# Kernel tuning notes

Measured on AMD Instinct MI355X. Metric: run time of the kernel, lower is better.

Reference implementation:

```python
import jax, jax.numpy as jnp
import numpy as np

N_SYM, N_DIS, F_IN, HID, OUT, E = 50000, 10000, 128, 128, 64, 640000
NEG_SLOPE = 0.2


def _gat(x_src, x_dst, src, dst, Ws, Wd, a_s, a_d, b, n_dst):
    # PyG GATConv (bipartite, heads=1, add_self_loops=False)
    h_src = x_src @ Ws                      # [Ns, H]
    h_dst = x_dst @ Wd                      # [Nd, H]
    al = h_src @ a_s                        # [Ns]
    ar = h_dst @ a_d                        # [Nd]
    e = jax.nn.leaky_relu(al[src] + ar[dst], NEG_SLOPE)   # [E]
    m = jax.ops.segment_max(e, dst, num_segments=n_dst)   # per-dst max
    ex = jnp.exp(e - m[dst])
    den = jax.ops.segment_sum(ex, dst, num_segments=n_dst)
    alpha = ex / den[dst]                   # segment softmax over in-edges
    out = jax.ops.segment_sum(alpha[:, None] * h_src[src], dst, num_segments=n_dst)
    return out + b


def setup_inputs() -> dict:
    key = jax.random.key(0)
    ks = jax.random.split(key, 16)
    s = 0.05
    return {
        'x_sym': jax.random.normal(ks[0], (N_SYM, F_IN), jnp.float32),
        'x_dis': jax.random.normal(ks[1], (N_DIS, F_IN), jnp.float32),
        'edge_src': jax.random.randint(ks[2], (E,), 0, N_SYM, jnp.int32),
        'edge_dst': jax.random.randint(ks[3], (E,), 0, N_DIS, jnp.int32),
        'Wsrc_sd': jax.random.normal(ks[4], (F_IN, HID), jnp.float32) * s,
        'Wdst_sd': jax.random.normal(ks[5], (F_IN, HID), jnp.float32) * s,
        'asrc_sd': jax.random.normal(ks[6], (HID,), jnp.float32) * s,
        'adst_sd': jax.random.normal(ks[7], (HID,), jnp.float32) * s,
        'b_sd': jax.random.normal(ks[8], (HID,), jnp.float32) * s,
        'Wsrc_ds': jax.random.normal(ks[9], (F_IN, HID), jnp.float32) * s,
        'Wdst_ds': jax.random.normal(ks[10], (F_IN, HID), jnp.float32) * s,
        'asrc_ds': jax.random.normal(ks[11], (HID,), jnp.float32) * s,
        'adst_ds': jax.random.normal(ks[12], (HID,), jnp.float32) * s,
        'b_ds': jax.random.normal(ks[13], (HID,), jnp.float32) * s,
        'lin_W': jax.random.normal(ks[14], (HID, OUT), jnp.float32) * s,
        'lin_b': jax.random.normal(ks[15], (OUT,), jnp.float32) * s,
    }


def reference(x_sym, x_dis, edge_src, edge_dst,
              Wsrc_sd, Wdst_sd, asrc_sd, adst_sd, b_sd,
              Wsrc_ds, Wdst_ds, asrc_ds, adst_ds, b_ds,
              lin_W, lin_b):
    # symptom -> disease edge type
    h_dis = _gat(x_sym, x_dis, edge_src, edge_dst,
                 Wsrc_sd, Wdst_sd, asrc_sd, adst_sd, b_sd, N_DIS)
    # disease -> symptom (reverse edges)
    h_sym = _gat(x_dis, x_sym, edge_dst, edge_src,
                 Wsrc_ds, Wdst_ds, asrc_ds, adst_ds, b_ds, N_SYM)
    h_sym = jax.nn.relu(h_sym)  # only symptom branch feeds lin
    return h_sym @ lin_W + lin_b
```

## Files before the change

### kernel.cpp

```cpp
#include <hip/hip_runtime.h>
#include <hip/hip_fp16.h>

#define N_SYM 50000
#define N_DIS 10000
#define F_IN 128
#define HID 128
#define OUTF 64
#define NE 640000
#define NEG_SLOPE 0.2f

#define SPAN 128
#define NB 391
#define SUBS 16
#define SCAP 192
#define CURSTRIDE 16
#define NREG (NB * SUBS)
#define LCAP 48

typedef _Float16 f16x8 __attribute__((ext_vector_type(8)));
typedef float f32x4 __attribute__((ext_vector_type(4)));

#define R1 16
__global__ __launch_bounds__(256) void k_proj(const float* __restrict__ x,
                                              const float* __restrict__ W,
                                              const float* __restrict__ asrc,
                                              const float* __restrict__ Wd,
                                              const float* __restrict__ ad,
                                              __half* __restrict__ h,
                                              float* __restrict__ al2,
                                              float* __restrict__ v_dst,
                                              int* __restrict__ bcur) {
    int tid = threadIdx.x;
    if (blockIdx.x == 625) {
        int k = tid >> 1;
        int hh = tid & 1;
        const float4* Wr = (const float4*)(Wd + k * HID + hh * 64);
        const float4* av = (const float4*)(ad + hh * 64);
        float s = 0.f;
#pragma unroll
        for (int j = 0; j < 16; ++j) {
            float4 w = Wr[j], xx = av[j];
            s += w.x * xx.x + w.y * xx.y + w.z * xx.z + w.w * xx.w;
        }
        s += __shfl_xor(s, 1);
        if (!hh) v_dst[k] = s;
        return;
    }
    int gid = blockIdx.x * 256 + tid;
    if (gid < NREG * CURSTRIDE) bcur[gid] = 0;
    __shared__ float xl[R1 * F_IN];
    int rowbase = blockIdx.x * R1;
    const float4* src = (const float4*)(x + rowbase * F_IN);
    float4* dl = (float4*)xl;
    for (int i = tid; i < R1 * F_IN / 4; i += 256) dl[i] = src[i];
    __syncthreads();
    int c2 = tid & 63;
    int rg = tid >> 6;
    float acc[4][2] = {};
    for (int k = 0; k < F_IN; ++k) {
        float2 w = *(const float2*)(W + k * HID + c2 * 2);
#pragma unroll
        for (int i = 0; i < 4; ++i) {
            float xv = xl[(rg + 4 * i) * F_IN + k];
            acc[i][0] += xv * w.x;
            acc[i][1] += xv * w.y;
        }
    }
    __half2* h2 = (__half2*)h;
    float2 av = *(const float2*)(asrc + 2 * c2);
#pragma unroll
    for (int i = 0; i < 4; ++i) {
        h2[(rowbase + rg + 4 * i) * 64 + c2] = __floats2half2_rn(acc[i][0], acc[i][1]);
        float p = acc[i][0] * av.x + acc[i][1] * av.y;
#pragma unroll
        for (int m = 32; m; m >>= 1) p += __shfl_xor(p, m);
        if (c2 == 0) al2[rowbase + rg + 4 * i] = p;
    }
}

__global__ __launch_bounds__(256) void k_ar(const float* __restrict__ h,
                                            const float* __restrict__ a,
                                            float* __restrict__ o,
                                            const int* __restrict__ esrc,
                                            const int* __restrict__ edst,
                                            int* __restrict__ bcur,
                                            unsigned int* __restrict__ bins) {
    int gid = blockIdx.x * 256 + threadIdx.x;
    if (gid < NE) {
        int s = esrc[gid];
        int d = edst[gid];
        int region = (s >> 7) * SUBS + (blockIdx.x & (SUBS - 1));
        unsigned int v = ((unsigned int)(s & 127) << 14) | (unsigned int)d;
        int pos = atomicAdd(&bcur[region * CURSTRIDE], 1);
        if (pos < SCAP) bins[region * SCAP + pos] = v;
    }
    int r = gid >> 5;
    int l = threadIdx.x & 31;
    if (r >= N_SYM) return;
    float4 hv = *(const float4*)(h + r * F_IN + l * 4);
    float4 av = *(const float4*)(a + l * 4);
    float s = hv.x * av.x + hv.y * av.y + hv.z * av.z + hv.w * av.w;
#pragma unroll
    for (int m = 16; m; m >>= 1) s += __shfl_xor(s, m);
    if (!l) o[r] = s;
}

__global__ __launch_bounds__(256) void k_build(const unsigned int* __restrict__ bins,
                                               const int* __restrict__ bcur,
                                               unsigned short* __restrict__ bucket,
                                               int* __restrict__ deg) {
    __shared__ int lcount[SPAN];
    __shared__ unsigned short lb[SPAN * LCAP];
    int tid = threadIdx.x;
    int bin = blockIdx.x;
    int nodebase = bin * SPAN;
    int nnodes = min(SPAN, N_SYM - nodebase);
    for (int i = tid; i < SPAN; i += 256) lcount[i] = 0;
    __syncthreads();
    int hw = tid >> 5;
    int hl = tid & 31;
    for (int sub = hw; sub < SUBS; sub += 8) {
        int region = bin * SUBS + sub;
        int n = bcur[region * CURSTRIDE];
        if (n > SCAP) n = SCAP;
        const unsigned int* base = bins + region * SCAP;
        for (int i = hl; i < n; i += 32) {
            unsigned int v = base[i];
            int sl = v >> 14;
            int d = v & 0x3FFF;
            int rank = atomicAdd(&lcount[sl], 1);
            if (rank < LCAP) lb[sl * LCAP + rank] = (unsigned short)d;
        }
    }
    __syncthreads();
    for (int i = tid; i < nnodes; i += 256)
        deg[nodebase + i] = min(lcount[i], LCAP);
    unsigned int* gb = (unsigned int*)(bucket + nodebase * LCAP);
    const unsigned int* lbu = (const unsigned int*)lb;
    int words = nnodes * LCAP / 2;
    for (int i = tid; i < words; i += 256) gb[i] = lbu[i];
}

__device__ __forceinline__ void acc_row(float4& acc, float2 rr, float ww) {
    __half2 a01 = *(__half2*)&rr.x;
    __half2 a23 = *(__half2*)&rr.y;
    float2 f01 = __half22float2(a01), f23 = __half22float2(a23);
    acc.x += ww * f01.x;
    acc.y += ww * f01.y;
    acc.z += ww * f23.x;
    acc.w += ww * f23.y;
}

__global__ __launch_bounds__(256) void k_agg(const int* __restrict__ deg,
                                             const unsigned short* __restrict__ bucket,
                                             const float* __restrict__ al2,
                                             const float* __restrict__ ar2,
                                             const __half* __restrict__ h16,
                                             const float* __restrict__ b,
                                             __half* __restrict__ hout) {
    int node = (blockIdx.x * 256 + threadIdx.x) >> 5;
    int l = threadIdx.x & 31;
    if (node >= N_SYM) return;
    int dg = deg[node];
    int off = node * LCAP;
    float arn = ar2[node];
    int di = 0;
    float lv = -1e30f;
    if (l < dg) {
        di = bucket[off + l];
        float t = al2[di] + arn;
        lv = (t > 0.f) ? t : NEG_SLOPE * t;
    }
    float mm = lv;
    for (int i = 32 + l; i < dg; i += 32) {
        float t = al2[bucket[off + i]] + arn;
        t = (t > 0.f) ? t : NEG_SLOPE * t;
        mm = fmaxf(mm, t);
    }
#pragma unroll
    for (int s = 16; s; s >>= 1) mm = fmaxf(mm, __shfl_xor(mm, s, 32));

    const float2* hb = (const float2*)h16;
    float4 acc = make_float4(0.f, 0.f, 0.f, 0.f);
    float den = 0.f;
    int dgc = dg < 32 ? dg : 32;
    int e = 0;
    for (; e + 4 <= dgc; e += 4) {
        int d0 = __shfl(di, e + 0, 32); float w0 = __expf(__shfl(lv, e + 0, 32) - mm);
        int d1 = __shfl(di, e + 1, 32); float w1 = __expf(__shfl(lv, e + 1, 32) - mm);
        int d2 = __shfl(di, e + 2, 32); float w2 = __expf(__shfl(lv, e + 2, 32) - mm);
        int d3 = __shfl(di, e + 3, 32); float w3 = __expf(__shfl(lv, e + 3, 32) - mm);
        float2 r0 = hb[d0 * 32 + l];
        float2 r1 = hb[d1 * 32 + l];
        float2 r2 = hb[d2 * 32 + l];
        float2 r3 = hb[d3 * 32 + l];
        den += w0 + w1 + w2 + w3;
        acc_row(acc, r0, w0);
        acc_row(acc, r1, w1);
        acc_row(acc, r2, w2);
        acc_row(acc, r3, w3);
    }
    for (; e < dgc; ++e) {
        int d = __shfl(di, e, 32);
        float w = __expf(__shfl(lv, e, 32) - mm);
        float2 r = hb[d * 32 + l];
        den += w;
        acc_row(acc, r, w);
    }
    for (int i = 32; i < dg; ++i) {
        int dd = bucket[off + i];
        float t = al2[dd] + arn;
        t = (t > 0.f) ? t : NEG_SLOPE * t;
        float w = __expf(t - mm);
        float2 r = hb[dd * 32 + l];
        den += w;
        acc_row(acc, r, w);
    }
    float inv = (dg > 0) ? 1.f / den : 0.f;
    float4 bv = *(const float4*)(b + l * 4);
    __half2 o01 = __floats2half2_rn(fmaxf(acc.x * inv + bv.x, 0.f),
                                    fmaxf(acc.y * inv + bv.y, 0.f));
    __half2 o23 = __floats2half2_rn(fmaxf(acc.z * inv + bv.z, 0.f),
                                    fmaxf(acc.w * inv + bv.w, 0.f));
    float2 pack;
    *(__half2*)&pack.x = o01;
    *(__half2*)&pack.y = o23;
    *(float2*)((__half2*)hout + node * 64 + 2 * l) = pack;
}

__global__ __launch_bounds__(256) void k_final(const __half* __restrict__ h,
                                               const float* __restrict__ W,
                                               const float* __restrict__ b,
                                               float* __restrict__ out) {
    __shared__ __align__(16) _Float16 BT[64][136];
    __shared__ float bias[64];
    int tid = threadIdx.x;
    for (int idx = tid; idx < HID * OUTF; idx += 256) {
        int k = idx >> 6, c = idx & 63;
        BT[c][k] = (_Float16)W[idx];
    }
    if (tid < 64) bias[tid] = b[tid];
    __syncthreads();
    int wave = tid >> 6, lane = tid & 63;
    int rowbase = blockIdx.x * 64 + wave * 16;
    int arow = rowbase + (lane & 15);
    if (arow >= N_SYM) arow = N_SYM - 1;
    int kbase = (lane >> 4) * 8;
    const _Float16* hp = (const _Float16*)h;
    f16x8 a[4];
#pragma unroll
    for (int kc = 0; kc < 4; ++kc)
        a[kc] = *(const f16x8*)(hp + arow * HID + kc * 32 + kbase);
#pragma unroll
    for (int ct = 0; ct < 4; ++ct) {
        int bcol = ct * 16 + (lane & 15);
        f32x4 acc = {0.f, 0.f, 0.f, 0.f};
#pragma unroll
        for (int kc = 0; kc < 4; ++kc) {
            f16x8 bf = *(const f16x8*)(&BT[bcol][kc * 32 + kbase]);
            acc = __builtin_amdgcn_mfma_f32_16x16x32_f16(a[kc], bf, acc, 0, 0, 0);
        }
        int r0 = rowbase + (lane >> 4) * 4;
        float bc = bias[bcol];
#pragma unroll
        for (int r = 0; r < 4; ++r) {
            int row = r0 + r;
            if (row < N_SYM) out[row * OUTF + bcol] = acc[r] + bc;
        }
    }
}

extern "C" void kernel_launch(void* const* d_in, const int* in_sizes, int n_in,
                              void* d_out, int out_size, void* d_ws, size_t ws_size,
                              hipStream_t stream) {
    const float* x_sym   = (const float*)d_in[0];
    const float* x_dis   = (const float*)d_in[1];
    const int*   esrc    = (const int*)d_in[2];
    const int*   edst    = (const int*)d_in[3];
    const float* Wsrc_ds = (const float*)d_in[9];
    const float* Wdst_ds = (const float*)d_in[10];
    const float* asrc_ds = (const float*)d_in[11];
    const float* adst_ds = (const float*)d_in[12];
    const float* b_ds    = (const float*)d_in[13];
    const float* lin_W   = (const float*)d_in[14];
    const float* lin_b   = (const float*)d_in[15];
    float* out = (float*)d_out;

    float*  ws     = (float*)d_ws;
    float*  v_dst  = ws;
    float*  al2    = v_dst + 128;
    float*  ar2    = al2 + N_DIS;
    int*    deg    = (int*)(ar2 + N_SYM);
    int*    bcur   = deg + N_SYM;
    unsigned int*   bins   = (unsigned int*)(bcur + NREG * CURSTRIDE);
    unsigned short* bucket = (unsigned short*)(bins + NREG * SCAP);
    __half* h16    = (__half*)(bucket + N_SYM * LCAP);
    __half* h_sym  = h16 + N_DIS * HID;

    k_proj<<<626, 256, 0, stream>>>(x_dis, Wsrc_ds, asrc_ds, Wdst_ds, adst_ds,
                                    h16, al2, v_dst, bcur);
    k_ar<<<N_SYM * 32 / 256, 256, 0, stream>>>(x_sym, v_dst, ar2, esrc, edst,
                                               bcur, bins);
    k_build<<<NB, 256, 0, stream>>>(bins, bcur, bucket, deg);
    k_agg<<<N_SYM * 32 / 256, 256, 0, stream>>>(deg, bucket, al2, ar2, h16,
                                                b_ds, h_sym);
    k_final<<<(N_SYM + 63) / 64, 256, 0, stream>>>(h_sym, lin_W, lin_b, out);
}
```

Baseline: 91.85 us.

## Fuse bucket build, attention aggregation and final linear into one kernel

```diff
diff --git a/kernel.cpp b/kernel.cpp
--- a/kernel.cpp
+++ b/kernel.cpp
@@ -16,22 +16,22 @@
 #define CURSTRIDE 16
 #define NREG (NB * SUBS)
 #define LCAP 48
+#define HSTR 144
+
+#define AR_BLOCKS 6250
+#define PROJ_BLOCKS 625
 
 typedef _Float16 f16x8 __attribute__((ext_vector_type(8)));
 typedef float f32x4 __attribute__((ext_vector_type(4)));
 
-#define R1 16
-__global__ __launch_bounds__(256) void k_proj(const float* __restrict__ x,
-                                              const float* __restrict__ W,
-                                              const float* __restrict__ asrc,
-                                              const float* __restrict__ Wd,
-                                              const float* __restrict__ ad,
-                                              __half* __restrict__ h,
-                                              float* __restrict__ al2,
-                                              float* __restrict__ v_dst,
-                                              int* __restrict__ bcur) {
+__global__ __launch_bounds__(256) void k_pre(const float* __restrict__ Wd,
+                                             const float* __restrict__ ad,
+                                             float* __restrict__ v_dst,
+                                             int* __restrict__ bcur) {
     int tid = threadIdx.x;
-    if (blockIdx.x == 625) {
+    for (int i = blockIdx.x * 256 + tid; i < NREG * CURSTRIDE; i += 64 * 256)
+        bcur[i] = 0;
+    if (blockIdx.x == 0) {
         int k = tid >> 1;
         int hh = tid & 1;
         const float4* Wr = (const float4*)(Wd + k * HID + hh * 64);
@@ -44,13 +44,48 @@
         }
         s += __shfl_xor(s, 1);
         if (!hh) v_dst[k] = s;
+    }
+}
+
+#define R1 16
+__global__ __launch_bounds__(256) void k_main(const float* __restrict__ x_sym,
+                                              const float* __restrict__ x_dis,
+                                              const int* __restrict__ esrc,
+                                              const int* __restrict__ edst,
+                                              const float* __restrict__ Wsrc,
+                                              const float* __restrict__ asrc,
+                                              const float* __restrict__ v_dst,
+                                              __half* __restrict__ h16,
+                                              float* __restrict__ al2,
+                                              float* __restrict__ ar2,
+                                              int* __restrict__ bcur,
+                                              unsigned int* __restrict__ bins) {
+    int tid = threadIdx.x;
+    if (blockIdx.x < AR_BLOCKS) {
+        int gid = blockIdx.x * 256 + tid;
+        if (gid < NE) {
+            int s = esrc[gid];
+            int d = edst[gid];
+            int region = (s >> 7) * SUBS + (blockIdx.x & (SUBS - 1));
+            unsigned int v = ((unsigned int)(s & 127) << 14) | (unsigned int)d;
+            int pos = atomicAdd(&bcur[region * CURSTRIDE], 1);
+            if (pos < SCAP) bins[region * SCAP + pos] = v;
+        }
+        int r = gid >> 5;
+        int l = tid & 31;
+        if (r >= N_SYM) return;
+        float4 hv = *(const float4*)(x_sym + r * F_IN + l * 4);
+        float4 av = *(const float4*)(v_dst + l * 4);
+        float s = hv.x * av.x + hv.y * av.y + hv.z * av.z + hv.w * av.w;
+#pragma unroll
+        for (int m = 16; m; m >>= 1) s += __shfl_xor(s, m);
+        if (!l) ar2[r] = s;
         return;
     }
-    int gid = blockIdx.x * 256 + tid;
-    if (gid < NREG * CURSTRIDE) bcur[gid] = 0;
+    int pblk = blockIdx.x - AR_BLOCKS;
     __shared__ float xl[R1 * F_IN];
-    int rowbase = blockIdx.x * R1;
-    const float4* src = (const float4*)(x + rowbase * F_IN);
+    int rowbase = pblk * R1;
+    const float4* src = (const float4*)(x_dis + rowbase * F_IN);
     float4* dl = (float4*)xl;
     for (int i = tid; i < R1 * F_IN / 4; i += 256) dl[i] = src[i];
     __syncthreads();
@@ -58,7 +93,7 @@
     int rg = tid >> 6;
     float acc[4][2] = {};
     for (int k = 0; k < F_IN; ++k) {
-        float2 w = *(const float2*)(W + k * HID + c2 * 2);
+        float2 w = *(const float2*)(Wsrc + k * HID + c2 * 2);
 #pragma unroll
         for (int i = 0; i < 4; ++i) {
             float xv = xl[(rg + 4 * i) * F_IN + k];
@@ -66,7 +101,7 @@
             acc[i][1] += xv * w.y;
         }
     }
-    __half2* h2 = (__half2*)h;
+    __half2* h2 = (__half2*)h16;
     float2 av = *(const float2*)(asrc + 2 * c2);
 #pragma unroll
     for (int i = 0; i < 4; ++i) {
@@ -78,49 +113,45 @@
     }
 }
 
-__global__ __launch_bounds__(256) void k_ar(const float* __restrict__ h,
-                                            const float* __restrict__ a,
-                                            float* __restrict__ o,
-                                            const int* __restrict__ esrc,
-                                            const int* __restrict__ edst,
-                                            int* __restrict__ bcur,
-                                            unsigned int* __restrict__ bins) {
-    int gid = blockIdx.x * 256 + threadIdx.x;
-    if (gid < NE) {
-        int s = esrc[gid];
-        int d = edst[gid];
-        int region = (s >> 7) * SUBS + (blockIdx.x & (SUBS - 1));
-        unsigned int v = ((unsigned int)(s & 127) << 14) | (unsigned int)d;
-        int pos = atomicAdd(&bcur[region * CURSTRIDE], 1);
-        if (pos < SCAP) bins[region * SCAP + pos] = v;
-    }
-    int r = gid >> 5;
-    int l = threadIdx.x & 31;
-    if (r >= N_SYM) return;
-    float4 hv = *(const float4*)(h + r * F_IN + l * 4);
-    float4 av = *(const float4*)(a + l * 4);
-    float s = hv.x * av.x + hv.y * av.y + hv.z * av.z + hv.w * av.w;
-#pragma unroll
-    for (int m = 16; m; m >>= 1) s += __shfl_xor(s, m);
-    if (!l) o[r] = s;
-}
-
-__global__ __launch_bounds__(256) void k_build(const unsigned int* __restrict__ bins,
-                                               const int* __restrict__ bcur,
-                                               unsigned short* __restrict__ bucket,
-                                               int* __restrict__ deg) {
+__device__ __forceinline__ void acc_row(float4& acc, float2 rr, float ww) {
+    __half2 a01 = *(__half2*)&rr.x;
+    __half2 a23 = *(__half2*)&rr.y;
+    float2 f01 = __half22float2(a01), f23 = __half22float2(a23);
+    acc.x += ww * f01.x;
+    acc.y += ww * f01.y;
+    acc.z += ww * f23.x;
+    acc.w += ww * f23.y;
+}
+
+__global__ __launch_bounds__(512) void k_fuse(const unsigned int* __restrict__ bins,
+                                              const int* __restrict__ bcur,
+                                              const float* __restrict__ al2,
+                                              const float* __restrict__ ar2,
+                                              const __half* __restrict__ h16,
+                                              const float* __restrict__ b_ds,
+                                              const float* __restrict__ lin_W,
+                                              const float* __restrict__ lin_b,
+                                              float* __restrict__ out) {
     __shared__ int lcount[SPAN];
     __shared__ unsigned short lb[SPAN * LCAP];
+    __shared__ __align__(16) _Float16 htile[SPAN][HSTR];
+    __shared__ __align__(16) _Float16 BT[OUTF][HSTR];
+    __shared__ float bias[OUTF];
     int tid = threadIdx.x;
     int bin = blockIdx.x;
     int nodebase = bin * SPAN;
     int nnodes = min(SPAN, N_SYM - nodebase);
-    for (int i = tid; i < SPAN; i += 256) lcount[i] = 0;
-    __syncthreads();
-    int hw = tid >> 5;
-    int hl = tid & 31;
-    for (int sub = hw; sub < SUBS; sub += 8) {
-        int region = bin * SUBS + sub;
+    for (int i = tid; i < SPAN; i += 512) lcount[i] = 0;
+    for (int idx = tid; idx < HID * OUTF; idx += 512) {
+        int k = idx >> 6, c = idx & 63;
+        BT[c][k] = (_Float16)lin_W[idx];
+    }
+    if (tid < OUTF) bias[tid] = lin_b[tid];
+    __syncthreads();
+    {
+        int hw = tid >> 5;
+        int hl = tid & 31;
+        int region = bin * SUBS + hw;
         int n = bcur[region * CURSTRIDE];
         if (n > SCAP) n = SCAP;
         const unsigned int* base = bins + region * SCAP;
@@ -133,124 +164,82 @@
         }
     }
     __syncthreads();
-    for (int i = tid; i < nnodes; i += 256)
-        deg[nodebase + i] = min(lcount[i], LCAP);
-    unsigned int* gb = (unsigned int*)(bucket + nodebase * LCAP);
-    const unsigned int* lbu = (const unsigned int*)lb;
-    int words = nnodes * LCAP / 2;
-    for (int i = tid; i < words; i += 256) gb[i] = lbu[i];
-}
-
-__device__ __forceinline__ void acc_row(float4& acc, float2 rr, float ww) {
-    __half2 a01 = *(__half2*)&rr.x;
-    __half2 a23 = *(__half2*)&rr.y;
-    float2 f01 = __half22float2(a01), f23 = __half22float2(a23);
-    acc.x += ww * f01.x;
-    acc.y += ww * f01.y;
-    acc.z += ww * f23.x;
-    acc.w += ww * f23.y;
-}
-
-__global__ __launch_bounds__(256) void k_agg(const int* __restrict__ deg,
-                                             const unsigned short* __restrict__ bucket,
-                                             const float* __restrict__ al2,
-                                             const float* __restrict__ ar2,
-                                             const __half* __restrict__ h16,
-                                             const float* __restrict__ b,
-                                             __half* __restrict__ hout) {
-    int node = (blockIdx.x * 256 + threadIdx.x) >> 5;
-    int l = threadIdx.x & 31;
-    if (node >= N_SYM) return;
-    int dg = deg[node];
-    int off = node * LCAP;
-    float arn = ar2[node];
-    int di = 0;
-    float lv = -1e30f;
-    if (l < dg) {
-        di = bucket[off + l];
-        float t = al2[di] + arn;
-        lv = (t > 0.f) ? t : NEG_SLOPE * t;
-    }
-    float mm = lv;
-    for (int i = 32 + l; i < dg; i += 32) {
-        float t = al2[bucket[off + i]] + arn;
-        t = (t > 0.f) ? t : NEG_SLOPE * t;
-        mm = fmaxf(mm, t);
-    }
-#pragma unroll
-    for (int s = 16; s; s >>= 1) mm = fmaxf(mm, __shfl_xor(mm, s, 32));
-
+    int wave = tid >> 6, lane = tid & 63, half = lane >> 5, l = lane & 31;
     const float2* hb = (const float2*)h16;
-    float4 acc = make_float4(0.f, 0.f, 0.f, 0.f);
-    float den = 0.f;
-    int dgc = dg < 32 ? dg : 32;
-    int e = 0;
-    for (; e + 4 <= dgc; e += 4) {
-        int d0 = __shfl(di, e + 0, 32); float w0 = __expf(__shfl(lv, e + 0, 32) - mm);
-        int d1 = __shfl(di, e + 1, 32); float w1 = __expf(__shfl(lv, e + 1, 32) - mm);
-        int d2 = __shfl(di, e + 2, 32); float w2 = __expf(__shfl(lv, e + 2, 32) - mm);
-        int d3 = __shfl(di, e + 3, 32); float w3 = __expf(__shfl(lv, e + 3, 32) - mm);
-        float2 r0 = hb[d0 * 32 + l];
-        float2 r1 = hb[d1 * 32 + l];
-        float2 r2 = hb[d2 * 32 + l];
-        float2 r3 = hb[d3 * 32 + l];
-        den += w0 + w1 + w2 + w3;
-        acc_row(acc, r0, w0);
-        acc_row(acc, r1, w1);
-        acc_row(acc, r2, w2);
-        acc_row(acc, r3, w3);
-    }
-    for (; e < dgc; ++e) {
-        int d = __shfl(di, e, 32);
-        float w = __expf(__shfl(lv, e, 32) - mm);
-        float2 r = hb[d * 32 + l];
-        den += w;
-        acc_row(acc, r, w);
-    }
-    for (int i = 32; i < dg; ++i) {
-        int dd = bucket[off + i];
-        float t = al2[dd] + arn;
-        t = (t > 0.f) ? t : NEG_SLOPE * t;
-        float w = __expf(t - mm);
-        float2 r = hb[dd * 32 + l];
-        den += w;
-        acc_row(acc, r, w);
-    }
-    float inv = (dg > 0) ? 1.f / den : 0.f;
-    float4 bv = *(const float4*)(b + l * 4);
-    __half2 o01 = __floats2half2_rn(fmaxf(acc.x * inv + bv.x, 0.f),
-                                    fmaxf(acc.y * inv + bv.y, 0.f));
-    __half2 o23 = __floats2half2_rn(fmaxf(acc.z * inv + bv.z, 0.f),
-                                    fmaxf(acc.w * inv + bv.w, 0.f));
-    float2 pack;
-    *(__half2*)&pack.x = o01;
-    *(__half2*)&pack.y = o23;
-    *(float2*)((__half2*)hout + node * 64 + 2 * l) = pack;
-}
-
-__global__ __launch_bounds__(256) void k_final(const __half* __restrict__ h,
-                                               const float* __restrict__ W,
-                                               const float* __restrict__ b,
-                                               float* __restrict__ out) {
-    __shared__ __align__(16) _Float16 BT[64][136];
-    __shared__ float bias[64];
-    int tid = threadIdx.x;
-    for (int idx = tid; idx < HID * OUTF; idx += 256) {
-        int k = idx >> 6, c = idx & 63;
-        BT[c][k] = (_Float16)W[idx];
-    }
-    if (tid < 64) bias[tid] = b[tid];
-    __syncthreads();
-    int wave = tid >> 6, lane = tid & 63;
-    int rowbase = blockIdx.x * 64 + wave * 16;
-    int arow = rowbase + (lane & 15);
-    if (arow >= N_SYM) arow = N_SYM - 1;
+    for (int p = 0; p < 8; ++p) {
+        int nl = p * 16 + wave * 2 + half;
+        if (nl >= nnodes) continue;
+        int dg = min(lcount[nl], LCAP);
+        int off = nl * LCAP;
+        float arn = ar2[nodebase + nl];
+        int di = 0;
+        float lv = -1e30f;
+        if (l < dg) {
+            di = lb[off + l];
+            float t = al2[di] + arn;
+            lv = (t > 0.f) ? t : NEG_SLOPE * t;
+        }
+        float mm = lv;
+        for (int i = 32 + l; i < dg; i += 32) {
+            float t = al2[lb[off + i]] + arn;
+            t = (t > 0.f) ? t : NEG_SLOPE * t;
+            mm = fmaxf(mm, t);
+        }
+#pragma unroll
+        for (int s = 16; s; s >>= 1) mm = fmaxf(mm, __shfl_xor(mm, s, 32));
+        float4 acc = make_float4(0.f, 0.f, 0.f, 0.f);
+        float den = 0.f;
+        int dgc = dg < 32 ? dg : 32;
+        int e = 0;
+        for (; e + 4 <= dgc; e += 4) {
+            int d0 = __shfl(di, e + 0, 32); float w0 = __expf(__shfl(lv, e + 0, 32) - mm);
+            int d1 = __shfl(di, e + 1, 32); float w1 = __expf(__shfl(lv, e + 1, 32) - mm);
+            int d2 = __shfl(di, e + 2, 32); float w2 = __expf(__shfl(lv, e + 2, 32) - mm);
+            int d3 = __shfl(di, e + 3, 32); float w3 = __expf(__shfl(lv, e + 3, 32) - mm);
+            float2 r0 = hb[d0 * 32 + l];
+            float2 r1 = hb[d1 * 32 + l];
+            float2 r2 = hb[d2 * 32 + l];
+            float2 r3 = hb[d3 * 32 + l];
+            den += w0 + w1 + w2 + w3;
+            acc_row(acc, r0, w0);
+            acc_row(acc, r1, w1);
+            acc_row(acc, r2, w2);
+            acc_row(acc, r3, w3);
+        }
+        for (; e < dgc; ++e) {
+            int d = __shfl(di, e, 32);
+            float w = __expf(__shfl(lv, e, 32) - mm);
+            float2 r = hb[d * 32 + l];
+            den += w;
+            acc_row(acc, r, w);
+        }
+        for (int i = 32; i < dg; ++i) {
+            int dd = lb[off + i];
+            float t = al2[dd] + arn;
+            t = (t > 0.f) ? t : NEG_SLOPE * t;
+            float w = __expf(t - mm);
+            float2 r = hb[dd * 32 + l];
+            den += w;
+            acc_row(acc, r, w);
+        }
+        float inv = (dg > 0) ? 1.f / den : 0.f;
+        float4 bv = *(const float4*)(b_ds + l * 4);
+        __half2 o01 = __floats2half2_rn(fmaxf(acc.x * inv + bv.x, 0.f),
+                                        fmaxf(acc.y * inv + bv.y, 0.f));
+        __half2 o23 = __floats2half2_rn(fmaxf(acc.z * inv + bv.z, 0.f),
+                                        fmaxf(acc.w * inv + bv.w, 0.f));
+        float2 pack;
+        *(__half2*)&pack.x = o01;
+        *(__half2*)&pack.y = o23;
+        *(float2*)&htile[nl][l * 4] = pack;
+    }
+    __syncthreads();
+    int rowloc = wave * 16 + (lane & 15);
     int kbase = (lane >> 4) * 8;
-    const _Float16* hp = (const _Float16*)h;
     f16x8 a[4];
 #pragma unroll
     for (int kc = 0; kc < 4; ++kc)
-        a[kc] = *(const f16x8*)(hp + arow * HID + kc * 32 + kbase);
+        a[kc] = *(const f16x8*)(&htile[rowloc][kc * 32 + kbase]);
 #pragma unroll
     for (int ct = 0; ct < 4; ++ct) {
         int bcol = ct * 16 + (lane & 15);
@@ -260,12 +249,12 @@
             f16x8 bf = *(const f16x8*)(&BT[bcol][kc * 32 + kbase]);
             acc = __builtin_amdgcn_mfma_f32_16x16x32_f16(a[kc], bf, acc, 0, 0, 0);
         }
-        int r0 = rowbase + (lane >> 4) * 4;
+        int r0 = wave * 16 + (lane >> 4) * 4;
         float bc = bias[bcol];
 #pragma unroll
         for (int r = 0; r < 4; ++r) {
-            int row = r0 + r;
-            if (row < N_SYM) out[row * OUTF + bcol] = acc[r] + bc;
+            int rl = r0 + r;
+            if (rl < nnodes) out[(nodebase + rl) * OUTF + bcol] = acc[r] + bc;
         }
     }
 }
@@ -290,19 +279,14 @@
     float*  v_dst  = ws;
     float*  al2    = v_dst + 128;
     float*  ar2    = al2 + N_DIS;
-    int*    deg    = (int*)(ar2 + N_SYM);
-    int*    bcur   = deg + N_SYM;
-    unsigned int*   bins   = (unsigned int*)(bcur + NREG * CURSTRIDE);
-    unsigned short* bucket = (unsigned short*)(bins + NREG * SCAP);
-    __half* h16    = (__half*)(bucket + N_SYM * LCAP);
-    __half* h_sym  = h16 + N_DIS * HID;
-
-    k_proj<<<626, 256, 0, stream>>>(x_dis, Wsrc_ds, asrc_ds, Wdst_ds, adst_ds,
-                                    h16, al2, v_dst, bcur);
-    k_ar<<<N_SYM * 32 / 256, 256, 0, stream>>>(x_sym, v_dst, ar2, esrc, edst,
-                                               bcur, bins);
-    k_build<<<NB, 256, 0, stream>>>(bins, bcur, bucket, deg);
-    k_agg<<<N_SYM * 32 / 256, 256, 0, stream>>>(deg, bucket, al2, ar2, h16,
-                                                b_ds, h_sym);
-    k_final<<<(N_SYM + 63) / 64, 256, 0, stream>>>(h_sym, lin_W, lin_b, out);
-}
+    int*    bcur   = (int*)(ar2 + N_SYM);
+    unsigned int* bins = (unsigned int*)(bcur + NREG * CURSTRIDE);
+    __half* h16    = (__half*)(bins + NREG * SCAP);
+
+    k_pre<<<64, 256, 0, stream>>>(Wdst_ds, adst_ds, v_dst, bcur);
+    k_main<<<AR_BLOCKS + PROJ_BLOCKS, 256, 0, stream>>>(x_sym, x_dis, esrc, edst,
+                                                        Wsrc_ds, asrc_ds, v_dst,
+                                                        h16, al2, ar2, bcur, bins);
+    k_fuse<<<NB, 512, 0, stream>>>(bins, bcur, al2, ar2, h16, b_ds,
+                                   lin_W, lin_b, out);
+}
```

Measured after the change: 95.63 us. +4.1%, slower.
